# Kernel tuning notes

Hardware: AMD Instinct MI355X
Metric: run time of the kernel (lower is better)

The kernel has to match this reference:

```python
import jax, jax.numpy as jnp
import numpy as np

STATE_DIM = 32
CONTROL_DIM = 8
EMBED_DIM = 96
LATENT_DIM = STATE_DIM + EMBED_DIM  # 128
HIDDEN = 512
B, M = 2048, 64


def setup_inputs() -> dict:
    key = jax.random.key(0)
    ks = jax.random.split(key, 16)
    s = lambda k, shp, fan: jax.random.normal(k, shp, jnp.float32) * (1.0 / np.sqrt(fan))
    return {
        "x_k": jax.random.normal(ks[0], (B, STATE_DIM), jnp.float32),
        "u_seq": jax.random.normal(ks[1], (B, M, CONTROL_DIM), jnp.float32),
        "x_next_seq": jax.random.normal(ks[2], (B, M, STATE_DIM), jnp.float32),
        # encoder MLP (depth=3): in->h, h->h, h->h, h->embed
        "W1": s(ks[3], (STATE_DIM, HIDDEN), STATE_DIM), "b1": jnp.zeros((HIDDEN,), jnp.float32),
        "W2": s(ks[4], (HIDDEN, HIDDEN), HIDDEN), "b2": jnp.zeros((HIDDEN,), jnp.float32),
        "W3": s(ks[5], (HIDDEN, HIDDEN), HIDDEN), "b3": jnp.zeros((HIDDEN,), jnp.float32),
        "Wo": s(ks[6], (HIDDEN, EMBED_DIM), HIDDEN), "bo": jnp.zeros((EMBED_DIM,), jnp.float32),
        # Koopman operators (Linear, no bias); stored as [in, out]
        "A": s(ks[7], (LATENT_DIM, LATENT_DIM), LATENT_DIM),
        "Bmat": s(ks[8], (CONTROL_DIM, LATENT_DIM), CONTROL_DIM),
    }


def _encode(x, W1, b1, W2, b2, W3, b3, Wo, bo):
    h = jax.nn.relu(x @ W1 + b1)
    h = jax.nn.relu(h @ W2 + b2)
    h = jax.nn.relu(h @ W3 + b3)
    return h @ Wo + bo


def _lift(x, W1, b1, W2, b2, W3, b3, Wo, bo):
    return jnp.concatenate([x, _encode(x, W1, b1, W2, b2, W3, b3, Wo, bo)], axis=-1)


def reference(x_k, u_seq, x_next_seq, W1, b1, W2, b2, W3, b3, Wo, bo, A, Bmat):
    m = u_seq.shape[1]
    z_k = _lift(x_k, W1, b1, W2, b2, W3, b3, Wo, bo)  # [B, L]
    # lift targets (encoder applied to flattened [B*M, S])
    z_target_seq = _lift(x_next_seq.reshape(-1, STATE_DIM), W1, b1, W2, b2, W3, b3, Wo, bo)
    z_target_seq = z_target_seq.reshape(-1, m, LATENT_DIM)
    # precompute control contributions, then sequential LTI recurrence via scan
    bu = jnp.einsum('bmc,cl->mbl', u_seq, Bmat)  # [M, B, L]

    def step(z, bu_i):
        z_next = z @ A + bu_i
        return z_next, z_next

    _, z_pred = jax.lax.scan(step, z_k, bu)  # [M, B, L]
    z_pred_seq = jnp.transpose(z_pred, (1, 0, 2))  # [B, M, L]
    x_pred_seq = z_pred_seq[..., :STATE_DIM]
    return (z_pred_seq, x_pred_seq, z_target_seq)
```

## Files before the change

kernel.cpp:

```cpp
#include <hip/hip_runtime.h>


typedef unsigned short u16;
typedef __attribute__((ext_vector_type(8))) short bf16x8;
typedef __attribute__((ext_vector_type(4))) short bf16x4;
typedef __attribute__((ext_vector_type(4))) float f32x4;

#define OFF_W1 0
#define OFF_W2 16384
#define OFF_W3 278528
#define OFF_WO 540672
#define OFF_ZK_BYTES 1179648
#define OFF_AH 1114112
#define OFF_AL 1130496

#define XPRED_OFF 16777216
#define ZTGT_OFF  20971520

__device__ __forceinline__ float bf2f(u16 u) {
  unsigned int i = ((unsigned int)u) << 16;
  return __builtin_bit_cast(float, i);
}
__device__ __forceinline__ u16 f2bf(float f) {
  unsigned int i = __builtin_bit_cast(unsigned int, f);
  i = (i + 0x7FFFu + ((i >> 16) & 1u)) >> 16;
  return (u16)i;
}

__global__ void prep_swizzle(const float* __restrict__ W1, const float* __restrict__ W2,
                             const float* __restrict__ W3, const float* __restrict__ Wo,
                             const float* __restrict__ Am, u16* __restrict__ dst) {
  int f = blockIdx.x;
  int l = threadIdx.x;
  const float* src; int K, N; u16* d; int lo = 0;
  if (f < 32)        { src = W1; K = 32;  N = 512; d = dst + OFF_W1; }
  else if (f < 544)  { src = W2; K = 512; N = 512; d = dst + OFF_W2; f -= 32; }
  else if (f < 1056) { src = W3; K = 512; N = 512; d = dst + OFF_W3; f -= 544; }
  else if (f < 1152) { src = Wo; K = 512; N = 96;  d = dst + OFF_WO; f -= 1056; }
  else if (f < 1184) { src = Am; K = 128; N = 128; d = dst + OFF_AH; f -= 1152; }
  else               { src = Am; K = 128; N = 128; d = dst + OFF_AL; f -= 1184; lo = 1; }
  const int KF = K >> 5;
  const int ct = f / KF, ks = f - ct * KF;
  const int q = l >> 4, n = l & 15;
  const int kbase = ks * 32 + q * 8;
  const int col = ct * 16 + n;
  bf16x8 vh;
  #pragma unroll
  for (int j = 0; j < 8; ++j) {
    float v = src[(size_t)(kbase + j) * N + col];
    u16 h = f2bf(v);
    if (lo) h = f2bf(v - bf2f(h));
    vh[j] = (short)h;
  }
  *(bf16x8*)(d + ((size_t)f * 64 + l) * 8) = vh;
}

__device__ __forceinline__ void store_h(const f32x4 (&acc)[4][8],
                                        const float* __restrict__ bias,
                                        u16* hbuf, int rh, int cg, int q, int n) {
  __syncthreads();
  #pragma unroll
  for (int i = 0; i < 8; ++i) {
    const int col = cg * 128 + i * 16 + n;
    const float bia = bias[col];
    #pragma unroll
    for (int rg = 0; rg < 4; ++rg) {
      const int rb = rh * 64 + rg * 16 + q * 4;
      float f0 = fmaxf(acc[rg][i][0] + bia, 0.f);
      float f1 = fmaxf(acc[rg][i][1] + bia, 0.f);
      float f2 = fmaxf(acc[rg][i][2] + bia, 0.f);
      float f3 = fmaxf(acc[rg][i][3] + bia, 0.f);
      unsigned p01, p23;
      asm("v_cvt_pk_bf16_f32 %0, %1, %2" : "=v"(p01) : "v"(f0), "v"(f1));
      asm("v_cvt_pk_bf16_f32 %0, %1, %2" : "=v"(p23) : "v"(f2), "v"(f3));
      hbuf[((rb + 0) * 512 + col) ^ (((rb + 0) & 7) << 3)] = (u16)(p01 & 0xFFFFu);
      hbuf[((rb + 1) * 512 + col) ^ (((rb + 1) & 7) << 3)] = (u16)(p01 >> 16);
      hbuf[((rb + 2) * 512 + col) ^ (((rb + 2) & 7) << 3)] = (u16)(p23 & 0xFFFFu);
      hbuf[((rb + 3) * 512 + col) ^ (((rb + 3) & 7) << 3)] = (u16)(p23 >> 16);
    }
  }
  __syncthreads();
}

__device__ __forceinline__ void big_layer(const u16* __restrict__ wb,
                                          const float* __restrict__ bias,
                                          u16* hbuf, int rh, int cg, int l, int q, int n) {
  f32x4 acc[4][8];
  #pragma unroll
  for (int rg = 0; rg < 4; ++rg)
    #pragma unroll
    for (int i = 0; i < 8; ++i) acc[rg][i] = (f32x4){0.f, 0.f, 0.f, 0.f};
  #pragma unroll 2
  for (int ks = 0; ks < 16; ++ks) {
    bf16x8 b[8], a[4];
    #pragma unroll
    for (int i = 0; i < 8; ++i)
      b[i] = *(const bf16x8*)(wb + (size_t)((8 * cg + i) * 16 + ks) * 512 + (size_t)l * 8);
    #pragma unroll
    for (int rg = 0; rg < 4; ++rg) {
      const int row = rh * 64 + rg * 16 + n;
      a[rg] = *(const bf16x8*)&hbuf[(row * 512 + ks * 32 + q * 8) ^ ((row & 7) << 3)];
    }
    #pragma unroll
    for (int rg = 0; rg < 4; ++rg)
      #pragma unroll
      for (int i = 0; i < 8; ++i)
        acc[rg][i] = __builtin_amdgcn_mfma_f32_16x16x32_bf16(a[rg], b[i], acc[rg][i], 0, 0, 0);
  }
  store_h(acc, bias, hbuf, rh, cg, q, n);
}

__global__ __launch_bounds__(512)
__attribute__((amdgpu_waves_per_eu(2, 2)))
void encoder_tgt(
    const float* __restrict__ xnext, const u16* __restrict__ wf,
    const float* __restrict__ b1, const float* __restrict__ b2,
    const float* __restrict__ b3, const float* __restrict__ bo_,
    float* __restrict__ ztgt) {
  __shared__ __align__(16) u16 hbuf[128 * 512];
  const int tid = threadIdx.x;
  const int wv = tid >> 6, l = tid & 63;
  const int q = l >> 4, n = l & 15;
  const int rh = wv >> 2, cg = wv & 3;
  const size_t row0 = (size_t)blockIdx.x * 128;

  {
    const int r = tid >> 2, k0 = (tid & 3) * 8;
    f32x4 x0 = *(const f32x4*)(xnext + (row0 + r) * 32 + k0);
    f32x4 x1 = *(const f32x4*)(xnext + (row0 + r) * 32 + k0 + 4);
    *(f32x4*)(ztgt + (row0 + r) * 128 + k0)     = x0;
    *(f32x4*)(ztgt + (row0 + r) * 128 + k0 + 4) = x1;
    bf16x8 v;
    #pragma unroll
    for (int j = 0; j < 4; ++j) { v[j] = (short)f2bf(x0[j]); v[4 + j] = (short)f2bf(x1[j]); }
    *(bf16x8*)&hbuf[(r * 512 + k0) ^ ((r & 7) << 3)] = v;
  }
  __syncthreads();

  {
    f32x4 acc[4][8];
    #pragma unroll
    for (int rg = 0; rg < 4; ++rg)
      #pragma unroll
      for (int i = 0; i < 8; ++i) acc[rg][i] = (f32x4){0.f, 0.f, 0.f, 0.f};
    bf16x8 a[4];
    #pragma unroll
    for (int rg = 0; rg < 4; ++rg) {
      const int row = rh * 64 + rg * 16 + n;
      a[rg] = *(const bf16x8*)&hbuf[(row * 512 + q * 8) ^ ((row & 7) << 3)];
    }
    #pragma unroll
    for (int i = 0; i < 8; ++i) {
      bf16x8 b = *(const bf16x8*)(wf + OFF_W1 + (size_t)(8 * cg + i) * 512 + (size_t)l * 8);
      #pragma unroll
      for (int rg = 0; rg < 4; ++rg)
        acc[rg][i] = __builtin_amdgcn_mfma_f32_16x16x32_bf16(a[rg], b, acc[rg][i], 0, 0, 0);
    }
    store_h(acc, b1, hbuf, rh, cg, q, n);
  }

  big_layer(wf + OFF_W2, b2, hbuf, rh, cg, l, q, n);
  big_layer(wf + OFF_W3, b3, hbuf, rh, cg, l, q, n);

  if (wv < 6) {
    f32x4 o[8];
    #pragma unroll
    for (int rg = 0; rg < 8; ++rg) o[rg] = (f32x4){0.f, 0.f, 0.f, 0.f};
    #pragma unroll 2
    for (int ks = 0; ks < 16; ++ks) {
      bf16x8 b = *(const bf16x8*)(wf + OFF_WO + (size_t)(wv * 16 + ks) * 512 + (size_t)l * 8);
      #pragma unroll
      for (int rg = 0; rg < 8; ++rg) {
        const int row = rg * 16 + n;
        bf16x8 a = *(const bf16x8*)&hbuf[(row * 512 + ks * 32 + q * 8) ^ ((row & 7) << 3)];
        o[rg] = __builtin_amdgcn_mfma_f32_16x16x32_bf16(a, b, o[rg], 0, 0, 0);
      }
    }
    const float bia = bo_[wv * 16 + n];
    #pragma unroll
    for (int rg = 0; rg < 8; ++rg)
      #pragma unroll
      for (int r = 0; r < 4; ++r)
        ztgt[(row0 + rg * 16 + q * 4 + r) * 128 + 32 + wv * 16 + n] = o[rg][r] + bia;
  }
}

__global__ __launch_bounds__(512) void encoder_zk_f32(
    const float* __restrict__ xk,
    const float* __restrict__ W1, const float* __restrict__ b1,
    const float* __restrict__ W2, const float* __restrict__ b2,
    const float* __restrict__ W3, const float* __restrict__ b3,
    const float* __restrict__ Wo, const float* __restrict__ bo_,
    float* __restrict__ zk_out) {
  __shared__ __align__(16) float hb[2][8][512];
  __shared__ __align__(16) float xb[8][32];
  const int t = threadIdx.x;
  const int row0 = blockIdx.x * 8;
  if (t < 256) {
    int r = t >> 5, j = t & 31;
    float v = xk[(size_t)(row0 + r) * 32 + j];
    xb[r][j] = v;
    zk_out[(size_t)(row0 + r) * 128 + j] = v;
  }
  __syncthreads();
  const int c = t;
  {
    float a[8];
    const float i0 = b1[c];
    #pragma unroll
    for (int r = 0; r < 8; ++r) a[r] = i0;
    for (int k = 0; k < 32; k += 4) {
      float w0 = W1[(size_t)(k+0)*512 + c];
      float w1 = W1[(size_t)(k+1)*512 + c];
      float w2 = W1[(size_t)(k+2)*512 + c];
      float w3 = W1[(size_t)(k+3)*512 + c];
      #pragma unroll
      for (int r = 0; r < 8; ++r) {
        f32x4 z = *(const f32x4*)&xb[r][k];
        a[r] += z[0]*w0 + z[1]*w1 + z[2]*w2 + z[3]*w3;
      }
    }
    #pragma unroll
    for (int r = 0; r < 8; ++r) hb[0][r][c] = fmaxf(a[r], 0.f);
  }
  __syncthreads();
  #pragma unroll
  for (int lyr = 0; lyr < 2; ++lyr) {
    const float* W = lyr ? W3 : W2;
    const float* bb = lyr ? b3 : b2;
    const float (*hin)[512] = hb[lyr & 1];
    float (*hout)[512] = hb[(lyr & 1) ^ 1];
    float a[8];
    const float i0 = bb[c];
    #pragma unroll
    for (int r = 0; r < 8; ++r) a[r] = i0;
    for (int k = 0; k < 512; k += 4) {
      float w0 = W[(size_t)(k+0)*512 + c];
      float w1 = W[(size_t)(k+1)*512 + c];
      float w2 = W[(size_t)(k+2)*512 + c];
      float w3 = W[(size_t)(k+3)*512 + c];
      #pragma unroll
      for (int r = 0; r < 8; ++r) {
        f32x4 z = *(const f32x4*)&hin[r][k];
        a[r] += z[0]*w0 + z[1]*w1 + z[2]*w2 + z[3]*w3;
      }
    }
    #pragma unroll
    for (int r = 0; r < 8; ++r) hout[r][c] = fmaxf(a[r], 0.f);
    __syncthreads();
  }
  if (t < 96) {
    float a[8];
    const float i0 = bo_[t];
    #pragma unroll
    for (int r = 0; r < 8; ++r) a[r] = i0;
    for (int k = 0; k < 512; k += 4) {
      float w0 = Wo[(size_t)(k+0)*96 + t];
      float w1 = Wo[(size_t)(k+1)*96 + t];
      float w2 = Wo[(size_t)(k+2)*96 + t];
      float w3 = Wo[(size_t)(k+3)*96 + t];
      #pragma unroll
      for (int r = 0; r < 8; ++r) {
        f32x4 z = *(const f32x4*)&hb[0][r][k];
        a[r] += z[0]*w0 + z[1]*w1 + z[2]*w2 + z[3]*w3;
      }
    }
    #pragma unroll
    for (int r = 0; r < 8; ++r)
      zk_out[(size_t)(row0 + r) * 128 + 32 + t] = a[r];
  }
}

__global__ __launch_bounds__(512) void scan_mfma(
    const float* __restrict__ zk, const u16* __restrict__ wf,
    const float* __restrict__ Bm, const float* __restrict__ useq,
    float* __restrict__ zpred, float* __restrict__ xpred) {
  __shared__ __align__(16) u16 ahf[32 * 512];
  __shared__ __align__(16) u16 alf[32 * 512];
  __shared__ __align__(16) float ubuf[8 * 512];
  __shared__ __align__(16) u16 zh[2][16][136];
  __shared__ __align__(16) u16 zl[2][16][136];
  const int t = threadIdx.x;
  const int wv = t >> 6, l = t & 63;
  const int q = l >> 4, n = l & 15;
  const size_t b0 = (size_t)blockIdx.x * 8;

  #pragma unroll
  for (int i = 0; i < 4; ++i) {
    const int f = wv * 4 + i;
    __builtin_amdgcn_global_load_lds(
        (const __attribute__((address_space(1))) unsigned int*)(wf + OFF_AH + (size_t)f * 512 + l * 8),
        (__attribute__((address_space(3))) unsigned int*)(ahf + (size_t)f * 512), 16, 0, 0);
    __builtin_amdgcn_global_load_lds(
        (const __attribute__((address_space(1))) unsigned int*)(wf + OFF_AL + (size_t)f * 512 + l * 8),
        (__attribute__((address_space(3))) unsigned int*)(alf + (size_t)f * 512), 16, 0, 0);
  }
  {
    const float* us = useq + b0 * 512;
    *(f32x4*)&ubuf[t * 8]     = *(const f32x4*)(us + t * 8);
    *(f32x4*)&ubuf[t * 8 + 4] = *(const f32x4*)(us + t * 8 + 4);
  }
  for (int i = t; i < 8 * 136; i += 512) {
    (&zh[0][8][0])[i] = 0; (&zh[1][8][0])[i] = 0;
    (&zl[0][8][0])[i] = 0; (&zl[1][8][0])[i] = 0;
  }
  if (t < 256) {
    const int r = t >> 5, c4 = (t & 31) * 4;
    f32x4 z = *(const f32x4*)(zk + (b0 + r) * 128 + c4);
    #pragma unroll
    for (int i = 0; i < 4; ++i) {
      u16 h = f2bf(z[i]);
      zh[0][r][c4 + i] = h;
      zl[0][r][c4 + i] = f2bf(z[i] - bf2f(h));
    }
  }
  const int myc = wv * 16 + n;
  float bmv[8];
  #pragma unroll
  for (int j = 0; j < 8; ++j) bmv[j] = Bm[(size_t)j * 128 + myc];
  __syncthreads();

  float bunow[4];
  #pragma unroll
  for (int r = 0; r < 4; ++r) {
    const int row = (q & 1) * 4 + r;
    f32x4 ua = *(const f32x4*)&ubuf[row * 512];
    f32x4 ub = *(const f32x4*)&ubuf[row * 512 + 4];
    bunow[r] = ua[0]*bmv[0] + ua[1]*bmv[1] + ua[2]*bmv[2] + ua[3]*bmv[3]
             + ub[0]*bmv[4] + ub[1]*bmv[5] + ub[2]*bmv[6] + ub[3]*bmv[7];
  }

  int cur = 0;
  for (int s = 0; s < 64; ++s) {
    f32x4 aH = {0.f, 0.f, 0.f, 0.f};
    f32x4 aL = {0.f, 0.f, 0.f, 0.f};
    f32x4 aM = {0.f, 0.f, 0.f, 0.f};
    #pragma unroll
    for (int ks = 0; ks < 4; ++ks) {
      const int ko = ks * 32 + q * 8;
      bf16x8 azh = *(const bf16x8*)&zh[cur][n][ko];
      bf16x8 azl = *(const bf16x8*)&zl[cur][n][ko];
      bf16x8 bh = *(const bf16x8*)&ahf[(size_t)(wv * 4 + ks) * 512 + l * 8];
      bf16x8 bl = *(const bf16x8*)&alf[(size_t)(wv * 4 + ks) * 512 + l * 8];
      aH = __builtin_amdgcn_mfma_f32_16x16x32_bf16(azh, bh, aH, 0, 0, 0);
      aL = __builtin_amdgcn_mfma_f32_16x16x32_bf16(azl, bh, aL, 0, 0, 0);
      aM = __builtin_amdgcn_mfma_f32_16x16x32_bf16(azh, bl, aM, 0, 0, 0);
    }
    f32x4 acc = aH + aL;
    acc = acc + aM;
    if (q < 2) {
      #pragma unroll
      for (int r = 0; r < 4; ++r) {
        const int row = q * 4 + r;
        const float v = acc[r] + bunow[r];
        u16 h = f2bf(v);
        zh[cur ^ 1][row][myc] = h;
        zl[cur ^ 1][row][myc] = f2bf(v - bf2f(h));
        const size_t go = (b0 + row) * 64 + s;
        zpred[go * 128 + myc] = v;
        if (wv < 2) xpred[go * 32 + myc] = v;
      }
    }
    if (s < 63) {
      #pragma unroll
      for (int r = 0; r < 4; ++r) {
        const int row = (q & 1) * 4 + r;
        f32x4 ua = *(const f32x4*)&ubuf[row * 512 + (s + 1) * 8];
        f32x4 ub = *(const f32x4*)&ubuf[row * 512 + (s + 1) * 8 + 4];
        bunow[r] = ua[0]*bmv[0] + ua[1]*bmv[1] + ua[2]*bmv[2] + ua[3]*bmv[3]
                 + ub[0]*bmv[4] + ub[1]*bmv[5] + ub[2]*bmv[6] + ub[3]*bmv[7];
      }
    }
    __syncthreads();
    cur ^= 1;
  }
}

extern "C" void kernel_launch(void* const* d_in, const int* in_sizes, int n_in,
                              void* d_out, int out_size, void* d_ws, size_t ws_size,
                              hipStream_t stream) {
  (void)in_sizes; (void)n_in; (void)out_size; (void)ws_size;
  const float* xk    = (const float*)d_in[0];
  const float* useq  = (const float*)d_in[1];
  const float* xnext = (const float*)d_in[2];
  const float* W1 = (const float*)d_in[3];
  const float* b1 = (const float*)d_in[4];
  const float* W2 = (const float*)d_in[5];
  const float* b2 = (const float*)d_in[6];
  const float* W3 = (const float*)d_in[7];
  const float* b3 = (const float*)d_in[8];
  const float* Wo = (const float*)d_in[9];
  const float* bo = (const float*)d_in[10];
  const float* A  = (const float*)d_in[11];
  const float* Bm = (const float*)d_in[12];

  float* out   = (float*)d_out;
  float* zpred = out;
  float* xpred = out + XPRED_OFF;
  float* ztgt  = out + ZTGT_OFF;
  u16*   wf    = (u16*)d_ws;
  float* zkw   = (float*)((char*)d_ws + OFF_ZK_BYTES);

  prep_swizzle<<<1216, 64, 0, stream>>>(W1, W2, W3, Wo, A, wf);
  encoder_zk_f32<<<256, 512, 0, stream>>>(xk, W1, b1, W2, b2, W3, b3, Wo, bo, zkw);
  scan_mfma<<<256, 512, 0, stream>>>(zkw, wf, Bm, useq, zpred, xpred);
  encoder_tgt<<<1024, 512, 0, stream>>>(xnext, wf, b1, b2, b3, bo, ztgt);
}
```

Before: 528.4 us.

## Switch target encoder to 32x32x16 MFMA with 64-row tiles and two blocks per CU

The target encoder now uses 32x32x16 bf16 MFMA instead of 16x16x32, and the weight pre-swizzle is rewritten to produce the 32-wide fragment layout. Each block processes 64 rows with 64 KB of LDS instead of 128 rows, and launch bounds request two blocks per CU, which doubles the grid. Each wave now covers 64 rows by 64 columns instead of 64 by 128. The aim is fewer MFMA issues per unit of work and better latency hiding through occupancy. The cost is that each block now reads the full weight set for only half as many rows, so weight reuse per block drops.

Result: faster. 493.8 us (-6.5%).

```diff
diff --git a/kernel.cpp b/kernel.cpp
--- a/kernel.cpp
+++ b/kernel.cpp
@@ -5,6 +5,7 @@
 typedef __attribute__((ext_vector_type(8))) short bf16x8;
 typedef __attribute__((ext_vector_type(4))) short bf16x4;
 typedef __attribute__((ext_vector_type(4))) float f32x4;
+typedef __attribute__((ext_vector_type(16))) float f32x16;
 
 #define OFF_W1 0
 #define OFF_W2 16384
@@ -32,156 +33,180 @@
                              const float* __restrict__ Am, u16* __restrict__ dst) {
   int f = blockIdx.x;
   int l = threadIdx.x;
-  const float* src; int K, N; u16* d; int lo = 0;
-  if (f < 32)        { src = W1; K = 32;  N = 512; d = dst + OFF_W1; }
-  else if (f < 544)  { src = W2; K = 512; N = 512; d = dst + OFF_W2; f -= 32; }
-  else if (f < 1056) { src = W3; K = 512; N = 512; d = dst + OFF_W3; f -= 544; }
-  else if (f < 1152) { src = Wo; K = 512; N = 96;  d = dst + OFF_WO; f -= 1056; }
-  else if (f < 1184) { src = Am; K = 128; N = 128; d = dst + OFF_AH; f -= 1152; }
-  else               { src = Am; K = 128; N = 128; d = dst + OFF_AL; f -= 1184; lo = 1; }
-  const int KF = K >> 5;
-  const int ct = f / KF, ks = f - ct * KF;
-  const int q = l >> 4, n = l & 15;
-  const int kbase = ks * 32 + q * 8;
-  const int col = ct * 16 + n;
-  bf16x8 vh;
-  #pragma unroll
-  for (int j = 0; j < 8; ++j) {
-    float v = src[(size_t)(kbase + j) * N + col];
-    u16 h = f2bf(v);
-    if (lo) h = f2bf(v - bf2f(h));
-    vh[j] = (short)h;
-  }
-  *(bf16x8*)(d + ((size_t)f * 64 + l) * 8) = vh;
-}
-
-__device__ __forceinline__ void store_h(const f32x4 (&acc)[4][8],
-                                        const float* __restrict__ bias,
-                                        u16* hbuf, int rh, int cg, int q, int n) {
-  __syncthreads();
-  #pragma unroll
-  for (int i = 0; i < 8; ++i) {
-    const int col = cg * 128 + i * 16 + n;
+  if (f < 1152) {
+    const float* src; int K, N; u16* d;
+    if (f < 32)        { src = W1; K = 32;  N = 512; d = dst + OFF_W1; }
+    else if (f < 544)  { src = W2; K = 512; N = 512; d = dst + OFF_W2; f -= 32; }
+    else if (f < 1056) { src = W3; K = 512; N = 512; d = dst + OFF_W3; f -= 544; }
+    else               { src = Wo; K = 512; N = 96;  d = dst + OFF_WO; f -= 1056; }
+    const int KF = K >> 4;
+    const int ct = f / KF, ks = f - ct * KF;
+    const int kbase = ks * 16 + (l >> 5) * 8;
+    const int col = ct * 32 + (l & 31);
+    bf16x8 vh;
+    #pragma unroll
+    for (int j = 0; j < 8; ++j)
+      vh[j] = (short)f2bf(src[(size_t)(kbase + j) * N + col]);
+    *(bf16x8*)(d + ((size_t)f * 64 + l) * 8) = vh;
+  } else {
+    int lo = 0; u16* d;
+    if (f < 1184) { d = dst + OFF_AH; f -= 1152; }
+    else          { d = dst + OFF_AL; f -= 1184; lo = 1; }
+    const int ct = f >> 2, ks = f & 3;
+    const int q = l >> 4, n = l & 15;
+    const int kbase = ks * 32 + q * 8;
+    const int col = ct * 16 + n;
+    bf16x8 vh;
+    #pragma unroll
+    for (int j = 0; j < 8; ++j) {
+      float v = Am[(size_t)(kbase + j) * 128 + col];
+      u16 h = f2bf(v);
+      if (lo) h = f2bf(v - bf2f(h));
+      vh[j] = (short)h;
+    }
+    *(bf16x8*)(d + ((size_t)f * 64 + l) * 8) = vh;
+  }
+}
+
+__device__ __forceinline__ void store_h32(const f32x16 (&acc)[2][2],
+                                          const float* __restrict__ bias,
+                                          u16* hbuf, int cg, int lo, int hi) {
+  __syncthreads();
+  #pragma unroll
+  for (int i = 0; i < 2; ++i) {
+    const int col = cg * 64 + i * 32 + lo;
     const float bia = bias[col];
     #pragma unroll
-    for (int rg = 0; rg < 4; ++rg) {
-      const int rb = rh * 64 + rg * 16 + q * 4;
-      float f0 = fmaxf(acc[rg][i][0] + bia, 0.f);
-      float f1 = fmaxf(acc[rg][i][1] + bia, 0.f);
-      float f2 = fmaxf(acc[rg][i][2] + bia, 0.f);
-      float f3 = fmaxf(acc[rg][i][3] + bia, 0.f);
-      unsigned p01, p23;
-      asm("v_cvt_pk_bf16_f32 %0, %1, %2" : "=v"(p01) : "v"(f0), "v"(f1));
-      asm("v_cvt_pk_bf16_f32 %0, %1, %2" : "=v"(p23) : "v"(f2), "v"(f3));
-      hbuf[((rb + 0) * 512 + col) ^ (((rb + 0) & 7) << 3)] = (u16)(p01 & 0xFFFFu);
-      hbuf[((rb + 1) * 512 + col) ^ (((rb + 1) & 7) << 3)] = (u16)(p01 >> 16);
-      hbuf[((rb + 2) * 512 + col) ^ (((rb + 2) & 7) << 3)] = (u16)(p23 & 0xFFFFu);
-      hbuf[((rb + 3) * 512 + col) ^ (((rb + 3) & 7) << 3)] = (u16)(p23 >> 16);
-    }
-  }
-  __syncthreads();
-}
-
-__device__ __forceinline__ void big_layer(const u16* __restrict__ wb,
-                                          const float* __restrict__ bias,
-                                          u16* hbuf, int rh, int cg, int l, int q, int n) {
-  f32x4 acc[4][8];
-  #pragma unroll
-  for (int rg = 0; rg < 4; ++rg)
-    #pragma unroll
-    for (int i = 0; i < 8; ++i) acc[rg][i] = (f32x4){0.f, 0.f, 0.f, 0.f};
-  #pragma unroll 2
-  for (int ks = 0; ks < 16; ++ks) {
-    bf16x8 b[8], a[4];
-    #pragma unroll
-    for (int i = 0; i < 8; ++i)
-      b[i] = *(const bf16x8*)(wb + (size_t)((8 * cg + i) * 16 + ks) * 512 + (size_t)l * 8);
-    #pragma unroll
-    for (int rg = 0; rg < 4; ++rg) {
-      const int row = rh * 64 + rg * 16 + n;
-      a[rg] = *(const bf16x8*)&hbuf[(row * 512 + ks * 32 + q * 8) ^ ((row & 7) << 3)];
-    }
-    #pragma unroll
-    for (int rg = 0; rg < 4; ++rg)
-      #pragma unroll
-      for (int i = 0; i < 8; ++i)
-        acc[rg][i] = __builtin_amdgcn_mfma_f32_16x16x32_bf16(a[rg], b[i], acc[rg][i], 0, 0, 0);
-  }
-  store_h(acc, bias, hbuf, rh, cg, q, n);
-}
-
-__global__ __launch_bounds__(512)
-__attribute__((amdgpu_waves_per_eu(2, 2)))
-void encoder_tgt(
+    for (int rg = 0; rg < 2; ++rg) {
+      #pragma unroll
+      for (int g = 0; g < 4; ++g) {
+        const int rb = rg * 32 + hi * 4 + g * 8;
+        float v0 = fmaxf(acc[rg][i][g * 4 + 0] + bia, 0.f);
+        float v1 = fmaxf(acc[rg][i][g * 4 + 1] + bia, 0.f);
+        float v2 = fmaxf(acc[rg][i][g * 4 + 2] + bia, 0.f);
+        float v3 = fmaxf(acc[rg][i][g * 4 + 3] + bia, 0.f);
+        unsigned p01, p23;
+        asm("v_cvt_pk_bf16_f32 %0, %1, %2" : "=v"(p01) : "v"(v0), "v"(v1));
+        asm("v_cvt_pk_bf16_f32 %0, %1, %2" : "=v"(p23) : "v"(v2), "v"(v3));
+        hbuf[((rb + 0) * 512 + col) ^ (((rb + 0) & 7) << 3)] = (u16)(p01 & 0xFFFFu);
+        hbuf[((rb + 1) * 512 + col) ^ (((rb + 1) & 7) << 3)] = (u16)(p01 >> 16);
+        hbuf[((rb + 2) * 512 + col) ^ (((rb + 2) & 7) << 3)] = (u16)(p23 & 0xFFFFu);
+        hbuf[((rb + 3) * 512 + col) ^ (((rb + 3) & 7) << 3)] = (u16)(p23 >> 16);
+      }
+    }
+  }
+  __syncthreads();
+}
+
+__device__ __forceinline__ void big_layer32(const u16* __restrict__ wb,
+                                            const float* __restrict__ bias,
+                                            u16* hbuf, int cg, int l, int lo, int hi) {
+  f32x16 acc[2][2];
+  #pragma unroll
+  for (int rg = 0; rg < 2; ++rg)
+    #pragma unroll
+    for (int i = 0; i < 2; ++i)
+      #pragma unroll
+      for (int e = 0; e < 16; ++e) acc[rg][i][e] = 0.f;
+  #pragma unroll 4
+  for (int ks = 0; ks < 32; ++ks) {
+    bf16x8 b[2], a[2];
+    #pragma unroll
+    for (int i = 0; i < 2; ++i)
+      b[i] = *(const bf16x8*)(wb + (size_t)((2 * cg + i) * 32 + ks) * 512 + (size_t)l * 8);
+    #pragma unroll
+    for (int rg = 0; rg < 2; ++rg) {
+      const int row = rg * 32 + lo;
+      a[rg] = *(const bf16x8*)&hbuf[(row * 512 + ks * 16 + hi * 8) ^ ((row & 7) << 3)];
+    }
+    #pragma unroll
+    for (int rg = 0; rg < 2; ++rg)
+      #pragma unroll
+      for (int i = 0; i < 2; ++i)
+        acc[rg][i] = __builtin_amdgcn_mfma_f32_32x32x16_bf16(a[rg], b[i], acc[rg][i], 0, 0, 0);
+  }
+  store_h32(acc, bias, hbuf, cg, lo, hi);
+}
+
+__global__ __launch_bounds__(512, 2) void encoder_tgt(
     const float* __restrict__ xnext, const u16* __restrict__ wf,
     const float* __restrict__ b1, const float* __restrict__ b2,
     const float* __restrict__ b3, const float* __restrict__ bo_,
     float* __restrict__ ztgt) {
-  __shared__ __align__(16) u16 hbuf[128 * 512];
+  __shared__ __align__(16) u16 hbuf[64 * 512];
   const int tid = threadIdx.x;
   const int wv = tid >> 6, l = tid & 63;
-  const int q = l >> 4, n = l & 15;
-  const int rh = wv >> 2, cg = wv & 3;
-  const size_t row0 = (size_t)blockIdx.x * 128;
+  const int lo = l & 31, hi = l >> 5;
+  const size_t row0 = (size_t)blockIdx.x * 64;
 
   {
-    const int r = tid >> 2, k0 = (tid & 3) * 8;
-    f32x4 x0 = *(const f32x4*)(xnext + (row0 + r) * 32 + k0);
-    f32x4 x1 = *(const f32x4*)(xnext + (row0 + r) * 32 + k0 + 4);
-    *(f32x4*)(ztgt + (row0 + r) * 128 + k0)     = x0;
-    *(f32x4*)(ztgt + (row0 + r) * 128 + k0 + 4) = x1;
-    bf16x8 v;
-    #pragma unroll
-    for (int j = 0; j < 4; ++j) { v[j] = (short)f2bf(x0[j]); v[4 + j] = (short)f2bf(x1[j]); }
-    *(bf16x8*)&hbuf[(r * 512 + k0) ^ ((r & 7) << 3)] = v;
+    const int r = tid >> 3, k0 = (tid & 7) * 4;
+    f32x4 x = *(const f32x4*)(xnext + (row0 + r) * 32 + k0);
+    *(f32x4*)(ztgt + (row0 + r) * 128 + k0) = x;
+    bf16x4 v;
+    #pragma unroll
+    for (int j = 0; j < 4; ++j) v[j] = (short)f2bf(x[j]);
+    *(bf16x4*)&hbuf[(r * 512 + k0) ^ ((r & 7) << 3)] = v;
   }
   __syncthreads();
 
   {
-    f32x4 acc[4][8];
-    #pragma unroll
-    for (int rg = 0; rg < 4; ++rg)
-      #pragma unroll
-      for (int i = 0; i < 8; ++i) acc[rg][i] = (f32x4){0.f, 0.f, 0.f, 0.f};
-    bf16x8 a[4];
-    #pragma unroll
-    for (int rg = 0; rg < 4; ++rg) {
-      const int row = rh * 64 + rg * 16 + n;
-      a[rg] = *(const bf16x8*)&hbuf[(row * 512 + q * 8) ^ ((row & 7) << 3)];
-    }
-    #pragma unroll
-    for (int i = 0; i < 8; ++i) {
-      bf16x8 b = *(const bf16x8*)(wf + OFF_W1 + (size_t)(8 * cg + i) * 512 + (size_t)l * 8);
-      #pragma unroll
-      for (int rg = 0; rg < 4; ++rg)
-        acc[rg][i] = __builtin_amdgcn_mfma_f32_16x16x32_bf16(a[rg], b, acc[rg][i], 0, 0, 0);
-    }
-    store_h(acc, b1, hbuf, rh, cg, q, n);
-  }
-
-  big_layer(wf + OFF_W2, b2, hbuf, rh, cg, l, q, n);
-  big_layer(wf + OFF_W3, b3, hbuf, rh, cg, l, q, n);
-
-  if (wv < 6) {
-    f32x4 o[8];
-    #pragma unroll
-    for (int rg = 0; rg < 8; ++rg) o[rg] = (f32x4){0.f, 0.f, 0.f, 0.f};
-    #pragma unroll 2
-    for (int ks = 0; ks < 16; ++ks) {
-      bf16x8 b = *(const bf16x8*)(wf + OFF_WO + (size_t)(wv * 16 + ks) * 512 + (size_t)l * 8);
-      #pragma unroll
-      for (int rg = 0; rg < 8; ++rg) {
-        const int row = rg * 16 + n;
-        bf16x8 a = *(const bf16x8*)&hbuf[(row * 512 + ks * 32 + q * 8) ^ ((row & 7) << 3)];
-        o[rg] = __builtin_amdgcn_mfma_f32_16x16x32_bf16(a, b, o[rg], 0, 0, 0);
-      }
-    }
-    const float bia = bo_[wv * 16 + n];
-    #pragma unroll
-    for (int rg = 0; rg < 8; ++rg)
-      #pragma unroll
-      for (int r = 0; r < 4; ++r)
-        ztgt[(row0 + rg * 16 + q * 4 + r) * 128 + 32 + wv * 16 + n] = o[rg][r] + bia;
+    f32x16 acc[2][2];
+    #pragma unroll
+    for (int rg = 0; rg < 2; ++rg)
+      #pragma unroll
+      for (int i = 0; i < 2; ++i)
+        #pragma unroll
+        for (int e = 0; e < 16; ++e) acc[rg][i][e] = 0.f;
+    #pragma unroll
+    for (int ks = 0; ks < 2; ++ks) {
+      bf16x8 b[2], a[2];
+      #pragma unroll
+      for (int i = 0; i < 2; ++i)
+        b[i] = *(const bf16x8*)(wf + OFF_W1 + (size_t)((2 * wv + i) * 2 + ks) * 512 + (size_t)l * 8);
+      #pragma unroll
+      for (int rg = 0; rg < 2; ++rg) {
+        const int row = rg * 32 + lo;
+        a[rg] = *(const bf16x8*)&hbuf[(row * 512 + ks * 16 + hi * 8) ^ ((row & 7) << 3)];
+      }
+      #pragma unroll
+      for (int rg = 0; rg < 2; ++rg)
+        #pragma unroll
+        for (int i = 0; i < 2; ++i)
+          acc[rg][i] = __builtin_amdgcn_mfma_f32_32x32x16_bf16(a[rg], b[i], acc[rg][i], 0, 0, 0);
+    }
+    store_h32(acc, b1, hbuf, wv, lo, hi);
+  }
+
+  big_layer32(wf + OFF_W2, b2, hbuf, wv, l, lo, hi);
+  big_layer32(wf + OFF_W3, b3, hbuf, wv, l, lo, hi);
+
+  if (wv < 3) {
+    f32x16 o[2];
+    #pragma unroll
+    for (int rg = 0; rg < 2; ++rg)
+      #pragma unroll
+      for (int e = 0; e < 16; ++e) o[rg][e] = 0.f;
+    #pragma unroll 4
+    for (int ks = 0; ks < 32; ++ks) {
+      bf16x8 b = *(const bf16x8*)(wf + OFF_WO + (size_t)(wv * 32 + ks) * 512 + (size_t)l * 8);
+      #pragma unroll
+      for (int rg = 0; rg < 2; ++rg) {
+        const int row = rg * 32 + lo;
+        bf16x8 a = *(const bf16x8*)&hbuf[(row * 512 + ks * 16 + hi * 8) ^ ((row & 7) << 3)];
+        o[rg] = __builtin_amdgcn_mfma_f32_32x32x16_bf16(a, b, o[rg], 0, 0, 0);
+      }
+    }
+    const float bia = bo_[wv * 32 + lo];
+    #pragma unroll
+    for (int rg = 0; rg < 2; ++rg)
+      #pragma unroll
+      for (int g = 0; g < 4; ++g)
+        #pragma unroll
+        for (int m = 0; m < 4; ++m) {
+          const int row = rg * 32 + hi * 4 + g * 8 + m;
+          ztgt[(row0 + row) * 128 + 32 + wv * 32 + lo] = o[rg][g * 4 + m] + bia;
+        }
   }
 }
 
@@ -404,5 +429,5 @@
   prep_swizzle<<<1216, 64, 0, stream>>>(W1, W2, W3, Wo, A, wf);
   encoder_zk_f32<<<256, 512, 0, stream>>>(xk, W1, b1, W2, b2, W3, b3, Wo, bo, zkw);
   scan_mfma<<<256, 512, 0, stream>>>(zkw, wf, Bm, useq, zpred, xpred);
-  encoder_tgt<<<1024, 512, 0, stream>>>(xnext, wf, b1, b2, b3, bo, ztgt);
-}
+  encoder_tgt<<<2048, 512, 0, stream>>>(xnext, wf, b1, b2, b3, bo, ztgt);
+}
```
